# Kernel optimization log

Measured on AMD Instinct MI355X. Metric: run time of the kernel, lower is better.

## Reference

```python
import jax, jax.numpy as jnp
import numpy as np

B, T, D = 128, 1024, 128
HS = [100, 100, 200, 200]  # stacked LSTM hidden sizes (from initialize_carry calls)
OUT = 6


def _lstm_layer(xs, Wx, Wh, b):
    """Flax-style LSTMCell scanned over time. xs: [B,T,Din] -> [B,T,H].
    Gates: i,f,g,o ; c' = sig(f)*c + sig(i)*tanh(g) ; h' = sig(o)*tanh(c')."""
    Bsz = xs.shape[0]
    H = Wh.shape[0]
    c0 = jnp.zeros((Bsz, H), xs.dtype)
    h0 = jnp.zeros((Bsz, H), xs.dtype)

    def step(carry, x_t):
        c, h = carry
        z = x_t @ Wx + h @ Wh + b  # [B, 4H]
        i, f, g, o = jnp.split(z, 4, axis=-1)
        c = jax.nn.sigmoid(f) * c + jax.nn.sigmoid(i) * jnp.tanh(g)
        h = jax.nn.sigmoid(o) * jnp.tanh(c)
        return (c, h), h

    (_, _), hs = jax.lax.scan(step, (c0, h0), jnp.swapaxes(xs, 0, 1))  # hs: [T,B,H]
    return jnp.swapaxes(hs, 0, 1)


def setup_inputs() -> dict:
    key = jax.random.key(0)
    ks = jax.random.split(key, 16)
    xs = jax.random.normal(ks[0], (B, T, D), dtype=jnp.float32)
    inp = {"xs": xs}
    d_in = D
    for li, H in enumerate(HS):
        s_x = 1.0 / np.sqrt(d_in)
        s_h = 1.0 / np.sqrt(H)
        inp[f"Wx{li}"] = jax.random.normal(ks[1 + 3 * li], (d_in, 4 * H), dtype=jnp.float32) * s_x
        inp[f"Wh{li}"] = jax.random.normal(ks[2 + 3 * li], (H, 4 * H), dtype=jnp.float32) * s_h
        inp[f"b{li}"] = jnp.zeros((4 * H,), dtype=jnp.float32)
        d_in = H
    inp["Wd"] = jax.random.normal(ks[13], (HS[-1], OUT), dtype=jnp.float32) / np.sqrt(HS[-1])
    inp["bd"] = jnp.zeros((OUT,), dtype=jnp.float32)
    return inp


def reference(xs, Wx0, Wh0, b0, Wx1, Wh1, b1, Wx2, Wh2, b2, Wx3, Wh3, b3, Wd, bd):
    # Four stacked scanned LSTM layers (dropout is identity in eval mode)
    h = _lstm_layer(xs, Wx0, Wh0, b0)
    h = _lstm_layer(h, Wx1, Wh1, b1)
    h = _lstm_layer(h, Wx2, Wh2, b2)
    h = _lstm_layer(h, Wx3, Wh3, b3)
    last = h[:, -1, :]  # [B, 200]
    return last @ Wd + bd  # [B, 6]
```

## Files before the change

### kernel.cpp

```cpp
#include <hip/hip_runtime.h>
#include <cstdint>
#include <cstddef>


#define AGENT __HIP_MEMORY_SCOPE_AGENT
#define FSTR 64

typedef __attribute__((ext_vector_type(8))) short  short8;
typedef __attribute__((ext_vector_type(4))) float  f32x4;

struct us4 { unsigned short x, y, z, w; };

__device__ __forceinline__ unsigned short f2bf(float x){
  unsigned u = __float_as_uint(x);
  unsigned r = u + 0x7FFFu + ((u >> 16) & 1u);
  return (unsigned short)(r >> 16);
}
__device__ __forceinline__ float bf2f(unsigned short h){
  return __uint_as_float(((unsigned)h) << 16);
}
__device__ __forceinline__ float sigmoidf_(float x){ return 1.f / (1.f + __expf(-x)); }

__device__ __forceinline__ void spin_ge(const unsigned* p, unsigned v){
  #pragma unroll 1
  for (int i = 0; i < 32; ++i){
    if (__hip_atomic_load(p, __ATOMIC_RELAXED, AGENT) >= v) return;
  }
  long s = 0;
  #pragma unroll 1
  while (__hip_atomic_load(p, __ATOMIC_RELAXED, AGENT) < v){
    __builtin_amdgcn_s_sleep(8);
    if (++s > (1L << 17)) break;
  }
}

__device__ __forceinline__ void load_hx(const unsigned* base, int w32, int loOff,
                                        short8& ah, short8& al){
  union U { unsigned long long q[2]; short8 v; } uh, ul;
  const unsigned long long* ph = (const unsigned long long*)(base + w32);
  const unsigned long long* pl = (const unsigned long long*)(base + loOff + w32);
  uh.q[0] = __hip_atomic_load(ph + 0, __ATOMIC_RELAXED, AGENT);
  uh.q[1] = __hip_atomic_load(ph + 1, __ATOMIC_RELAXED, AGENT);
  ul.q[0] = __hip_atomic_load(pl + 0, __ATOMIC_RELAXED, AGENT);
  ul.q[1] = __hip_atomic_load(pl + 1, __ATOMIC_RELAXED, AGENT);
  ah = uh.v; al = ul.v;
}

__global__ __launch_bounds__(256) void gemm_pregate(
    const float* __restrict__ A, const float* __restrict__ W,
    const float* __restrict__ bias, float* __restrict__ G,
    int K, int KT, int N, size_t strideT, size_t strideB)
{
  __shared__ unsigned short Ahi[256*40];
  __shared__ unsigned short Alo[256*40];
  __shared__ unsigned short Bhi[80*40];
  __shared__ unsigned short Blo[80*40];

  const int tid  = threadIdx.x;
  const int mb   = blockIdx.x;
  const int n0   = blockIdx.y * 80;
  const int wave = tid >> 6, lane = tid & 63;
  const int ln15 = lane & 15, quad = lane >> 4;

  f32x4 acc[4][5];
  for (int a = 0; a < 4; ++a)
    for (int b = 0; b < 5; ++b)
      acc[a][b] = (f32x4){0.f, 0.f, 0.f, 0.f};

  for (int kt = 0; kt < KT; ++kt){
    const int k0 = kt * 32;
    const bool full = (k0 + 31) < K;
    for (int i = 0; i < 8; ++i){
      const int e   = tid + 256*i;
      const int row = e >> 3, seg = e & 7;
      const int mm  = mb*256 + row;
      const float* rp = A + (size_t)(mm >> 7)*strideT + (size_t)(mm & 127)*strideB;
      const int k = k0 + seg*4;
      float v0, v1, v2, v3;
      if (full){
        float4 v = *(const float4*)(rp + k);
        v0 = v.x; v1 = v.y; v2 = v.z; v3 = v.w;
      } else {
        v0 = (k+0 < K) ? rp[k+0] : 0.f;
        v1 = (k+1 < K) ? rp[k+1] : 0.f;
        v2 = (k+2 < K) ? rp[k+2] : 0.f;
        v3 = (k+3 < K) ? rp[k+3] : 0.f;
      }
      const unsigned short h0=f2bf(v0), h1=f2bf(v1), h2=f2bf(v2), h3=f2bf(v3);
      us4 hv{h0, h1, h2, h3};
      us4 lv{f2bf(v0-bf2f(h0)), f2bf(v1-bf2f(h1)), f2bf(v2-bf2f(h2)), f2bf(v3-bf2f(h3))};
      *(us4*)&Ahi[row*40 + seg*4] = hv;
      *(us4*)&Alo[row*40 + seg*4] = lv;
    }
    for (int i = 0; i < 10; ++i){
      const int e  = tid + 256*i;
      const int kk = e / 80, nn = e - kk*80;
      const int k  = k0 + kk;
      const float v = (k < K) ? W[(size_t)k*N + n0 + nn] : 0.f;
      const unsigned short hb = f2bf(v);
      Bhi[nn*40 + kk] = hb;
      Blo[nn*40 + kk] = f2bf(v - bf2f(hb));
    }
    __syncthreads();
    short8 a_h[4], a_l[4];
    for (int mt = 0; mt < 4; ++mt){
      const int aoff = (wave*64 + mt*16 + ln15)*40 + quad*8;
      a_h[mt] = *(const short8*)&Ahi[aoff];
      a_l[mt] = *(const short8*)&Alo[aoff];
    }
    for (int nt = 0; nt < 5; ++nt){
      const int boff = (nt*16 + ln15)*40 + quad*8;
      const short8 b_h = *(const short8*)&Bhi[boff];
      const short8 b_l = *(const short8*)&Blo[boff];
      for (int mt = 0; mt < 4; ++mt){
        acc[mt][nt] = __builtin_amdgcn_mfma_f32_16x16x32_bf16(a_h[mt], b_h, acc[mt][nt], 0,0,0);
        acc[mt][nt] = __builtin_amdgcn_mfma_f32_16x16x32_bf16(a_l[mt], b_h, acc[mt][nt], 0,0,0);
        acc[mt][nt] = __builtin_amdgcn_mfma_f32_16x16x32_bf16(a_h[mt], b_l, acc[mt][nt], 0,0,0);
      }
    }
    __syncthreads();
  }
  for (int nt = 0; nt < 5; ++nt){
    const float bv = bias[n0 + nt*16 + ln15];
    for (int mt = 0; mt < 4; ++mt){
      const int mbase = mb*256 + wave*64 + mt*16 + quad*4;
      #pragma unroll
      for (int r = 0; r < 4; ++r)
        G[(size_t)(mbase + r)*N + n0 + nt*16 + ln15] = acc[mt][nt][r] + bv;
    }
  }
}

template<int H, int HP, int P, bool HAS_X>
__device__ __forceinline__ void rec_stage(
    const float* __restrict__ G0, const float* __restrict__ Wx,
    const float* __restrict__ Wh, const float* __restrict__ bias,
    int HprevReal,
    const unsigned* __restrict__ HxUp, unsigned* __restrict__ HxOwn,
    const unsigned* __restrict__ flgUp, unsigned* __restrict__ flgOwn,
    unsigned* __restrict__ flgDn, int PUp, int PDn,
    float* __restrict__ cstate, float* __restrict__ hlast,
    int g, int m, int t0, int TC, int Tlast, char* smem)
{
  constexpr int HHM  = H / P;
  constexpr int COLS = 4 * HHM;
  constexpr int CP   = COLS;
  constexpr int ZSTR = CP + 1;
  constexpr int KPo  = ((H + 31)/32)*32;
  constexpr int RSo  = KPo / 2;
  constexpr int RSp  = HP / 2;
  constexpr int KX   = HAS_X ? HP : 0;
  constexpr int KALL = KX + KPo;
  constexpr int KTX  = KX / 32;
  constexpr int KTH  = KPo / 32;
  constexpr int KSTR = KALL + 8;
  constexpr int NT   = CP / 16;
  constexpr int NE   = 16 * HHM / 2;
  constexpr int PR   = HHM / 2;
  constexpr int N4H  = 4 * H;
  constexpr int SLOTo = 2*16*RSo;
  constexpr int SLOTp = 2*16*RSp;

  unsigned short* whT_hi = (unsigned short*)smem;
  unsigned short* whT_lo = whT_hi + CP*KSTR;
  float* zbuf = (float*)(whT_lo + CP*KSTR);

  const int tid  = threadIdx.x;
  const int row0 = g * 16;
  const int lane = tid & 63, wave = tid >> 6;
  const int ln15 = lane & 15, quad = lane >> 4;

  for (int e = tid; e < COLS*KALL; e += 256){
    const int k = e / COLS, c = e - k*COLS;
    const int gate = c / HHM, hh = c - gate*HHM;
    const int col = gate*H + m*HHM + hh;
    float w = 0.f;
    if (HAS_X){
      if (k < KX){ if (k < HprevReal) w = Wx[(size_t)k*N4H + col]; }
      else { const int k2 = k - KX; if (k2 < H) w = Wh[(size_t)k2*N4H + col]; }
    } else {
      if (k < H) w = Wh[(size_t)k*N4H + col];
    }
    const unsigned short hi = f2bf(w);
    whT_hi[c*KSTR + k] = hi;
    whT_lo[c*KSTR + k] = f2bf(w - bf2f(hi));
  }

  const int r_g  = tid / PR;
  const int hh0  = 2*(tid - r_g*PR);
  const int kidx = m*HHM + hh0;
  float c0 = 0.f, c1 = 0.f;
  if (tid < NE && t0 > 0){
    const float2 cv = *(const float2*)&cstate[(size_t)(row0 + r_g)*H + kidx];
    c0 = cv.x; c1 = cv.y;
  }
  float2 bv[4] = {};
  if (HAS_X){
    if (tid < NE){
      #pragma unroll
      for (int gate = 0; gate < 4; ++gate)
        bv[gate] = *(const float2*)&bias[gate*H + kidx];
    }
  }
  __syncthreads();

  const int g16 = g*16;

  for (int tl = 0; tl < TC; ++tl){
    const int t = t0 + tl;

    float2 gv[4] = {};
    if constexpr (!HAS_X){
      if (tid < NE){
        const float* Gt = G0 + ((size_t)tl*128 + row0 + r_g)*(size_t)N4H + kidx;
        #pragma unroll
        for (int gate = 0; gate < 4; ++gate)
          gv[gate] = *(const float2*)(Gt + gate*H);
      }
    }

    if (HAS_X && wave == 0 && lane < PUp)
      spin_ge(&flgUp[(size_t)(g16 + lane)*FSTR], (unsigned)(t+1));
    if (PDn > 0 && t >= 8 && wave == 1 && lane < PDn)
      spin_ge(&flgDn[(size_t)(g16 + lane)*FSTR], (unsigned)(t-7));
    __syncthreads();

    f32x4 acc[2];
    acc[0] = (f32x4){0.f,0.f,0.f,0.f};
    acc[1] = (f32x4){0.f,0.f,0.f,0.f};
    auto do_tile = [&](const short8& a_h, const short8& a_l, int koW){
      #pragma unroll
      for (int s = 0; s < 2; ++s){
        const int nt = wave + 4*s;
        if (nt < NT){
          const int boff = (nt*16 + ln15)*KSTR + quad*8 + koW;
          const short8 b_h = *(const short8*)&whT_hi[boff];
          const short8 b_l = *(const short8*)&whT_lo[boff];
          acc[s] = __builtin_amdgcn_mfma_f32_16x16x32_bf16(a_h, b_h, acc[s], 0,0,0);
          acc[s] = __builtin_amdgcn_mfma_f32_16x16x32_bf16(a_l, b_h, acc[s], 0,0,0);
          acc[s] = __builtin_amdgcn_mfma_f32_16x16x32_bf16(a_h, b_l, acc[s], 0,0,0);
        }
      }
    };

    if constexpr (HAS_X){
      const unsigned* up = HxUp + ((size_t)(t & 7)*8 + g) * SLOTp;
      #pragma unroll
      for (int kt = 0; kt < KTX; ++kt){
        short8 a_h, a_l;
        load_hx(up, ln15*RSp + kt*16 + quad*4, 16*RSp, a_h, a_l);
        do_tile(a_h, a_l, kt*32);
      }
    }

    if (wave == 0 && lane < P)
      spin_ge(&flgOwn[(size_t)(g16 + lane)*FSTR], (unsigned)t);
    __syncthreads();

    {
      const unsigned* own = HxOwn + ((size_t)((t-1) & 7)*8 + g) * SLOTo;
      #pragma unroll
      for (int kt = 0; kt < KTH; ++kt){
        short8 a_h, a_l;
        load_hx(own, ln15*RSo + kt*16 + quad*4, 16*RSo, a_h, a_l);
        do_tile(a_h, a_l, KX + kt*32);
      }
    }
    {
      #pragma unroll
      for (int s = 0; s < 2; ++s){
        const int nt = wave + 4*s;
        if (nt < NT)
          #pragma unroll
          for (int r = 0; r < 4; ++r)
            zbuf[(quad*4 + r)*ZSTR + nt*16 + ln15] = acc[s][r];
      }
    }
    __syncthreads();

    if (tid < NE){
      const float* zr = zbuf + r_g*ZSTR;
      const float2 b0 = HAS_X ? bv[0] : gv[0];
      const float2 b1 = HAS_X ? bv[1] : gv[1];
      const float2 b2 = HAS_X ? bv[2] : gv[2];
      const float2 b3 = HAS_X ? bv[3] : gv[3];
      const float zi0 = zr[0*HHM + hh0]   + b0.x, zi1 = zr[0*HHM + hh0+1] + b0.y;
      const float zf0 = zr[1*HHM + hh0]   + b1.x, zf1 = zr[1*HHM + hh0+1] + b1.y;
      const float zg0 = zr[2*HHM + hh0]   + b2.x, zg1 = zr[2*HHM + hh0+1] + b2.y;
      const float zo0 = zr[3*HHM + hh0]   + b3.x, zo1 = zr[3*HHM + hh0+1] + b3.y;
      c0 = sigmoidf_(zf0)*c0 + sigmoidf_(zi0)*tanhf(zg0);
      c1 = sigmoidf_(zf1)*c1 + sigmoidf_(zi1)*tanhf(zg1);
      const float h0 = sigmoidf_(zo0)*tanhf(c0);
      const float h1 = sigmoidf_(zo1)*tanhf(c1);
      const unsigned short h0h = f2bf(h0), h1h = f2bf(h1);
      const unsigned short h0l = f2bf(h0 - bf2f(h0h)), h1l = f2bf(h1 - bf2f(h1h));
      const unsigned whi = ((unsigned)h1h << 16) | (unsigned)h0h;
      const unsigned wlo = ((unsigned)h1l << 16) | (unsigned)h0l;
      unsigned* dst = HxOwn + ((size_t)(t & 7)*8 + g) * SLOTo;
      const int w32 = r_g*RSo + (kidx >> 1);
      __hip_atomic_store(&dst[w32],          whi, __ATOMIC_RELAXED, AGENT);
      __hip_atomic_store(&dst[16*RSo + w32], wlo, __ATOMIC_RELAXED, AGENT);
      if (hlast && t == Tlast-1){
        float2 hv{h0, h1};
        *(float2*)&hlast[(size_t)(row0 + r_g)*H + kidx] = hv;
      }
    }
    __syncthreads();
    if (tid == 0)
      __hip_atomic_store(&flgOwn[(size_t)(g16 + m)*FSTR], (unsigned)(t+1),
                         __ATOMIC_RELAXED, AGENT);
  }

  if (tid < NE){
    float2 cv{c0, c1};
    *(float2*)&cstate[(size_t)(row0 + r_g)*H + kidx] = cv;
  }
}

struct FusedArgs {
  const float *G0;
  const float *Wx1, *Wx2, *Wx3;
  const float *Wh0, *Wh1, *Wh2, *Wh3;
  const float *b1, *b2, *b3;
  unsigned *Hx0, *Hx1, *Hx2, *Hx3;
  unsigned *flags;
  float *cst;
  float *hlast;
  int t0, TC, Tlast;
};

__global__ __launch_bounds__(256) void lstm_fused(FusedArgs a){
  extern __shared__ char smem[];
  const int b = blockIdx.x;
  constexpr int LF = 128*FSTR;
  if (b < 40){
    rec_stage<100, 0, 5, false>(a.G0, nullptr, a.Wh0, nullptr, 0,
        nullptr, a.Hx0, nullptr, a.flags + 0*LF, a.flags + 1*LF, 0, 5,
        a.cst + 0*128*200, nullptr, b & 7, b >> 3, a.t0, a.TC, a.Tlast, smem);
  } else if (b < 80){
    const int bb = b - 40;
    rec_stage<100, 128, 5, true>(nullptr, a.Wx1, a.Wh1, a.b1, 100,
        a.Hx0, a.Hx1, a.flags + 0*LF, a.flags + 1*LF, a.flags + 2*LF, 5, 10,
        a.cst + 1*128*200, nullptr, bb & 7, bb >> 3, a.t0, a.TC, a.Tlast, smem);
  } else if (b < 160){
    const int bb = b - 80;
    rec_stage<200, 128, 10, true>(nullptr, a.Wx2, a.Wh2, a.b2, 100,
        a.Hx1, a.Hx2, a.flags + 1*LF, a.flags + 2*LF, a.flags + 3*LF, 5, 10,
        a.cst + 2*128*200, nullptr, bb & 7, bb >> 3, a.t0, a.TC, a.Tlast, smem);
  } else {
    const int bb = b - 160;
    rec_stage<200, 224, 10, true>(nullptr, a.Wx3, a.Wh3, a.b3, 200,
        a.Hx2, a.Hx3, a.flags + 2*LF, a.flags + 3*LF, nullptr, 10, 0,
        a.cst + 3*128*200, a.hlast, bb & 7, bb >> 3, a.t0, a.TC, a.Tlast, smem);
  }
}

__global__ __launch_bounds__(256) void head_kernel(
    const float* __restrict__ hlast, const float* __restrict__ Wd,
    const float* __restrict__ bd, float* __restrict__ out)
{
  const int e = blockIdx.x*256 + threadIdx.x;
  if (e >= 128*6) return;
  const int b = e / 6, o = e - 6*b;
  float s = bd[o];
  const float* hp = hlast + (size_t)b*200;
  for (int k = 0; k < 200; ++k) s += hp[k] * Wd[k*6 + o];
  out[e] = s;
}

__global__ void fill_sentinel(float* out, int n){
  const int i = blockIdx.x*blockDim.x + threadIdx.x;
  if (i < n) out[i] = 1.0e30f;
}

extern "C" void kernel_launch(void* const* d_in, const int* in_sizes, int n_in,
                              void* d_out, int out_size, void* d_ws, size_t ws_size,
                              hipStream_t stream)
{
  (void)in_sizes; (void)n_in;
  const float* xs  = (const float*)d_in[0];
  const float* Wx[4] = {(const float*)d_in[1], (const float*)d_in[4],
                        (const float*)d_in[7], (const float*)d_in[10]};
  const float* Wh[4] = {(const float*)d_in[2], (const float*)d_in[5],
                        (const float*)d_in[8], (const float*)d_in[11]};
  const float* bs[4] = {(const float*)d_in[3], (const float*)d_in[6],
                        (const float*)d_in[9], (const float*)d_in[12]};
  const float* Wd = (const float*)d_in[13];
  const float* bd = (const float*)d_in[14];
  float* out = (float*)d_out;

  char* ws = (char*)d_ws;
  const size_t HXU[4] = {131072, 131072, 229376, 229376};
  const size_t HX_TOT = HXU[0]+HXU[1]+HXU[2]+HXU[3];
  const size_t FLAGS_BYTES = (size_t)4*128*FSTR*4;
  size_t off = 0;
  const size_t OFF_FLAGS = off; off += FLAGS_BYTES;
  const size_t OFF_HX    = off; off += HX_TOT*4;
  const size_t OFF_CST   = off; off += (size_t)4*128*200*4;
  const size_t OFF_HLAST = off; off += (size_t)128*200*4;
  off = (off + 255) & ~(size_t)255;
  const size_t FIXED_END = off;

  int CT = 0;
  for (int ct = 1024; ct >= 8; ct >>= 1){
    const size_t need = FIXED_END + (size_t)ct*128*400*4;
    if (ws_size >= need){ CT = ct; break; }
  }
  if (CT == 0){
    fill_sentinel<<<(out_size + 255)/256, 256, 0, stream>>>(out, out_size);
    return;
  }

  unsigned* flags = (unsigned*)(ws + OFF_FLAGS);
  unsigned* Hx0   = (unsigned*)(ws + OFF_HX);
  unsigned* Hx1   = Hx0 + HXU[0];
  unsigned* Hx2   = Hx1 + HXU[1];
  unsigned* Hx3   = Hx2 + HXU[2];
  float* cst      = (float*)(ws + OFF_CST);
  float* hlast    = (float*)(ws + OFF_HLAST);
  float* G0       = (float*)(ws + FIXED_END);

  const int FUSED_LDS = 151104;
  hipFuncSetAttribute(reinterpret_cast<const void*>(lstm_fused),
                      hipFuncAttributeMaxDynamicSharedMemorySize, FUSED_LDS);

  hipMemsetAsync(flags, 0, FLAGS_BYTES, stream);
  hipMemsetAsync(Hx0, 0, HX_TOT*4, stream);

  FusedArgs fa;
  fa.Wx1 = Wx[1]; fa.Wx2 = Wx[2]; fa.Wx3 = Wx[3];
  fa.Wh0 = Wh[0]; fa.Wh1 = Wh[1]; fa.Wh2 = Wh[2]; fa.Wh3 = Wh[3];
  fa.b1 = bs[1];  fa.b2 = bs[2];  fa.b3 = bs[3];
  fa.Hx0 = Hx0; fa.Hx1 = Hx1; fa.Hx2 = Hx2; fa.Hx3 = Hx3;
  fa.flags = flags; fa.cst = cst; fa.hlast = hlast;
  fa.G0 = G0; fa.Tlast = 1024;

  const int NC  = 1024 / CT;
  const int GMX = CT*128/256;
  for (int c = 0; c < NC; ++c){
    const int t0 = c*CT;
    gemm_pregate<<<dim3(GMX,5), 256, 0, stream>>>(xs + (size_t)t0*128, Wx[0], bs[0], G0,
        128, 4, 400, (size_t)128, (size_t)131072);
    fa.t0 = t0; fa.TC = CT;
    lstm_fused<<<240, 256, FUSED_LDS, stream>>>(fa);
  }

  head_kernel<<<3, 256, 0, stream>>>(hlast, Wd, bd, out);
}
```

Baseline: 6.527 ms.

## Split input projections of layers 1-3 into separate producer blocks

Adds dedicated pre_stage blocks that compute the Wx input projection plus bias for layers 1-3 into ring-buffered gate arrays. The recurrent blocks then only do the Wh matmul on the critical path, which shortens each serial timestep. Flag waits are spread across individual lanes with an acquire fence in place of __syncthreads, and the new flags signal to producers when ring slots can be reused. Block count rises from 240 to 440 and the LDS request is reduced so all blocks stay co-resident. The cost is extra global traffic for the gate arrays and more spin-wait synchronisation, with a deadlock risk if the blocks are not all resident at once.

```diff
diff --git a/kernel.cpp b/kernel.cpp
--- a/kernel.cpp
+++ b/kernel.cpp
@@ -131,56 +131,42 @@
   }
 }
 
-template<int H, int HP, int P, bool HAS_X>
-__device__ __forceinline__ void rec_stage(
-    const float* __restrict__ G0, const float* __restrict__ Wx,
-    const float* __restrict__ Wh, const float* __restrict__ bias,
-    int HprevReal,
-    const unsigned* __restrict__ HxUp, unsigned* __restrict__ HxOwn,
-    const unsigned* __restrict__ flgUp, unsigned* __restrict__ flgOwn,
-    unsigned* __restrict__ flgDn, int PUp, int PDn,
+template<int H, int P, bool GW>
+__device__ __forceinline__ void rec_stage2(
+    const float* __restrict__ Gsrc, const float* __restrict__ Wh,
+    unsigned* __restrict__ HxOwn,
+    unsigned* __restrict__ flgOwn, const unsigned* __restrict__ flgG,
+    const unsigned* __restrict__ flgDn, int PDn,
     float* __restrict__ cstate, float* __restrict__ hlast,
     int g, int m, int t0, int TC, int Tlast, char* smem)
 {
   constexpr int HHM  = H / P;
   constexpr int COLS = 4 * HHM;
-  constexpr int CP   = COLS;
-  constexpr int ZSTR = CP + 1;
+  constexpr int ZSTR = COLS + 1;
   constexpr int KPo  = ((H + 31)/32)*32;
   constexpr int RSo  = KPo / 2;
-  constexpr int RSp  = HP / 2;
-  constexpr int KX   = HAS_X ? HP : 0;
-  constexpr int KALL = KX + KPo;
-  constexpr int KTX  = KX / 32;
   constexpr int KTH  = KPo / 32;
-  constexpr int KSTR = KALL + 8;
-  constexpr int NT   = CP / 16;
+  constexpr int KSTR = KPo + 8;
+  constexpr int NT   = COLS / 16;
   constexpr int NE   = 16 * HHM / 2;
   constexpr int PR   = HHM / 2;
   constexpr int N4H  = 4 * H;
   constexpr int SLOTo = 2*16*RSo;
-  constexpr int SLOTp = 2*16*RSp;
 
   unsigned short* whT_hi = (unsigned short*)smem;
-  unsigned short* whT_lo = whT_hi + CP*KSTR;
-  float* zbuf = (float*)(whT_lo + CP*KSTR);
+  unsigned short* whT_lo = whT_hi + COLS*KSTR;
+  float* zbuf = (float*)(whT_lo + COLS*KSTR);
 
   const int tid  = threadIdx.x;
   const int row0 = g * 16;
   const int lane = tid & 63, wave = tid >> 6;
   const int ln15 = lane & 15, quad = lane >> 4;
 
-  for (int e = tid; e < COLS*KALL; e += 256){
+  for (int e = tid; e < COLS*KPo; e += 256){
     const int k = e / COLS, c = e - k*COLS;
     const int gate = c / HHM, hh = c - gate*HHM;
     const int col = gate*H + m*HHM + hh;
-    float w = 0.f;
-    if (HAS_X){
-      if (k < KX){ if (k < HprevReal) w = Wx[(size_t)k*N4H + col]; }
-      else { const int k2 = k - KX; if (k2 < H) w = Wh[(size_t)k2*N4H + col]; }
-    } else {
-      if (k < H) w = Wh[(size_t)k*N4H + col];
-    }
+    float w = (k < H) ? Wh[(size_t)k*N4H + col] : 0.f;
     const unsigned short hi = f2bf(w);
     whT_hi[c*KSTR + k] = hi;
     whT_lo[c*KSTR + k] = f2bf(w - bf2f(hi));
@@ -194,14 +180,6 @@
     const float2 cv = *(const float2*)&cstate[(size_t)(row0 + r_g)*H + kidx];
     c0 = cv.x; c1 = cv.y;
   }
-  float2 bv[4] = {};
-  if (HAS_X){
-    if (tid < NE){
-      #pragma unroll
-      for (int gate = 0; gate < 4; ++gate)
-        bv[gate] = *(const float2*)&bias[gate*H + kidx];
-    }
-  }
   __syncthreads();
 
   const int g16 = g*16;
@@ -209,85 +187,67 @@
   for (int tl = 0; tl < TC; ++tl){
     const int t = t0 + tl;
 
-    float2 gv[4] = {};
-    if constexpr (!HAS_X){
-      if (tid < NE){
-        const float* Gt = G0 + ((size_t)tl*128 + row0 + r_g)*(size_t)N4H + kidx;
-        #pragma unroll
-        for (int gate = 0; gate < 4; ++gate)
-          gv[gate] = *(const float2*)(Gt + gate*H);
-      }
-    }
-
-    if (HAS_X && wave == 0 && lane < PUp)
-      spin_ge(&flgUp[(size_t)(g16 + lane)*FSTR], (unsigned)(t+1));
-    if (PDn > 0 && t >= 8 && wave == 1 && lane < PDn)
-      spin_ge(&flgDn[(size_t)(g16 + lane)*FSTR], (unsigned)(t-7));
-    __syncthreads();
+    if (lane < P && lane != m)
+      spin_ge(&flgOwn[(size_t)(g16 + lane)*FSTR], (unsigned)t);
+    if (PDn > 0 && t >= 8 && lane >= 40 && lane < 40 + PDn)
+      spin_ge(&flgDn[(size_t)(g16 + (lane-40))*FSTR], (unsigned)(t-7));
+    if (GW && lane == 62)
+      spin_ge(&flgG[(size_t)(g16 + m)*FSTR], (unsigned)(t+1));
+    __builtin_amdgcn_fence(__ATOMIC_ACQUIRE, "agent");
+
+    float2 gv[4];
+    if (tid < NE){
+      const float* Gt = GW
+          ? Gsrc + ((size_t)(t & 7)*128 + row0 + r_g)*(size_t)N4H + kidx
+          : Gsrc + ((size_t)tl*128 + row0 + r_g)*(size_t)N4H + kidx;
+      #pragma unroll
+      for (int gate = 0; gate < 4; ++gate){
+        union { unsigned long long q; float2 f; } u;
+        u.q = __hip_atomic_load((const unsigned long long*)(Gt + gate*H),
+                                __ATOMIC_RELAXED, AGENT);
+        gv[gate] = u.f;
+      }
+    }
 
     f32x4 acc[2];
     acc[0] = (f32x4){0.f,0.f,0.f,0.f};
     acc[1] = (f32x4){0.f,0.f,0.f,0.f};
-    auto do_tile = [&](const short8& a_h, const short8& a_l, int koW){
-      #pragma unroll
-      for (int s = 0; s < 2; ++s){
-        const int nt = wave + 4*s;
-        if (nt < NT){
-          const int boff = (nt*16 + ln15)*KSTR + quad*8 + koW;
-          const short8 b_h = *(const short8*)&whT_hi[boff];
-          const short8 b_l = *(const short8*)&whT_lo[boff];
-          acc[s] = __builtin_amdgcn_mfma_f32_16x16x32_bf16(a_h, b_h, acc[s], 0,0,0);
-          acc[s] = __builtin_amdgcn_mfma_f32_16x16x32_bf16(a_l, b_h, acc[s], 0,0,0);
-          acc[s] = __builtin_amdgcn_mfma_f32_16x16x32_bf16(a_h, b_l, acc[s], 0,0,0);
-        }
-      }
-    };
-
-    if constexpr (HAS_X){
-      const unsigned* up = HxUp + ((size_t)(t & 7)*8 + g) * SLOTp;
-      #pragma unroll
-      for (int kt = 0; kt < KTX; ++kt){
-        short8 a_h, a_l;
-        load_hx(up, ln15*RSp + kt*16 + quad*4, 16*RSp, a_h, a_l);
-        do_tile(a_h, a_l, kt*32);
-      }
-    }
-
-    if (wave == 0 && lane < P)
-      spin_ge(&flgOwn[(size_t)(g16 + lane)*FSTR], (unsigned)t);
-    __syncthreads();
-
     {
       const unsigned* own = HxOwn + ((size_t)((t-1) & 7)*8 + g) * SLOTo;
       #pragma unroll
       for (int kt = 0; kt < KTH; ++kt){
         short8 a_h, a_l;
         load_hx(own, ln15*RSo + kt*16 + quad*4, 16*RSo, a_h, a_l);
-        do_tile(a_h, a_l, KX + kt*32);
-      }
-    }
-    {
-      #pragma unroll
-      for (int s = 0; s < 2; ++s){
-        const int nt = wave + 4*s;
-        if (nt < NT)
-          #pragma unroll
-          for (int r = 0; r < 4; ++r)
-            zbuf[(quad*4 + r)*ZSTR + nt*16 + ln15] = acc[s][r];
-      }
+        #pragma unroll
+        for (int s = 0; s < 2; ++s){
+          const int nt = wave + 4*s;
+          if (nt < NT){
+            const int boff = (nt*16 + ln15)*KSTR + quad*8 + kt*32;
+            const short8 b_h = *(const short8*)&whT_hi[boff];
+            const short8 b_l = *(const short8*)&whT_lo[boff];
+            acc[s] = __builtin_amdgcn_mfma_f32_16x16x32_bf16(a_h, b_h, acc[s], 0,0,0);
+            acc[s] = __builtin_amdgcn_mfma_f32_16x16x32_bf16(a_l, b_h, acc[s], 0,0,0);
+            acc[s] = __builtin_amdgcn_mfma_f32_16x16x32_bf16(a_h, b_l, acc[s], 0,0,0);
+          }
+        }
+      }
+    }
+    #pragma unroll
+    for (int s = 0; s < 2; ++s){
+      const int nt = wave + 4*s;
+      if (nt < NT)
+        #pragma unroll
+        for (int r = 0; r < 4; ++r)
+          zbuf[(quad*4 + r)*ZSTR + nt*16 + ln15] = acc[s][r];
     }
     __syncthreads();
 
     if (tid < NE){
       const float* zr = zbuf + r_g*ZSTR;
-      const float2 b0 = HAS_X ? bv[0] : gv[0];
-      const float2 b1 = HAS_X ? bv[1] : gv[1];
-      const float2 b2 = HAS_X ? bv[2] : gv[2];
-      const float2 b3 = HAS_X ? bv[3] : gv[3];
-      const float zi0 = zr[0*HHM + hh0]   + b0.x, zi1 = zr[0*HHM + hh0+1] + b0.y;
-      const float zf0 = zr[1*HHM + hh0]   + b1.x, zf1 = zr[1*HHM + hh0+1] + b1.y;
-      const float zg0 = zr[2*HHM + hh0]   + b2.x, zg1 = zr[2*HHM + hh0+1] + b2.y;
-      const float zo0 = zr[3*HHM + hh0]   + b3.x, zo1 = zr[3*HHM + hh0+1] + b3.y;
+      const float zi0 = zr[0*HHM + hh0]   + gv[0].x, zi1 = zr[0*HHM + hh0+1] + gv[0].y;
+      const float zf0 = zr[1*HHM + hh0]   + gv[1].x, zf1 = zr[1*HHM + hh0+1] + gv[1].y;
+      const float zg0 = zr[2*HHM + hh0]   + gv[2].x, zg1 = zr[2*HHM + hh0+1] + gv[2].y;
+      const float zo0 = zr[3*HHM + hh0]   + gv[3].x, zo1 = zr[3*HHM + hh0+1] + gv[3].y;
       c0 = sigmoidf_(zf0)*c0 + sigmoidf_(zi0)*tanhf(zg0);
       c1 = sigmoidf_(zf1)*c1 + sigmoidf_(zi1)*tanhf(zg1);
       const float h0 = sigmoidf_(zo0)*tanhf(c0);
@@ -317,12 +277,110 @@
   }
 }
 
+template<int H, int P, int HP, int Pprev>
+__device__ __forceinline__ void pre_stage(
+    const float* __restrict__ Wx, const float* __restrict__ bias, int HprevReal,
+    const unsigned* __restrict__ HxUp, float* __restrict__ Gdst,
+    const unsigned* __restrict__ flgUp, const unsigned* __restrict__ flgRec,
+    unsigned* __restrict__ flgPre,
+    int g, int m, int t0, int TC, char* smem)
+{
+  constexpr int HHM  = H / P;
+  constexpr int COLS = 4 * HHM;
+  constexpr int KSTR = HP + 8;
+  constexpr int KTX  = HP / 32;
+  constexpr int NT   = COLS / 16;
+  constexpr int N4H  = 4 * H;
+  constexpr int RSp  = HP / 2;
+  constexpr int SLOTp = 2*16*RSp;
+
+  unsigned short* wxT_hi = (unsigned short*)smem;
+  unsigned short* wxT_lo = wxT_hi + COLS*KSTR;
+
+  const int tid  = threadIdx.x;
+  const int lane = tid & 63, wave = tid >> 6;
+  const int ln15 = lane & 15, quad = lane >> 4;
+  const int g16  = g*16;
+
+  for (int e = tid; e < COLS*HP; e += 256){
+    const int k = e / COLS, c = e - k*COLS;
+    const int gate = c / HHM, hh = c - gate*HHM;
+    const int col = gate*H + m*HHM + hh;
+    float w = (k < HprevReal) ? Wx[(size_t)k*N4H + col] : 0.f;
+    const unsigned short hi = f2bf(w);
+    wxT_hi[c*KSTR + k] = hi;
+    wxT_lo[c*KSTR + k] = f2bf(w - bf2f(hi));
+  }
+
+  int cN[2]; float bN[2];
+  #pragma unroll
+  for (int s = 0; s < 2; ++s){
+    const int nt = wave + 4*s;
+    if (nt < NT){
+      const int sc = nt*16 + ln15;
+      const int gate = sc / HHM, hh = sc - gate*HHM;
+      cN[s] = gate*H + m*HHM + hh;
+      bN[s] = bias[cN[s]];
+    } else { cN[s] = 0; bN[s] = 0.f; }
+  }
+  __syncthreads();
+
+  for (int tl = 0; tl < TC; ++tl){
+    const int t = t0 + tl;
+
+    if (lane < Pprev)
+      spin_ge(&flgUp[(size_t)(g16 + lane)*FSTR], (unsigned)(t+1));
+    if (t >= 8 && lane == 62)
+      spin_ge(&flgRec[(size_t)(g16 + m)*FSTR], (unsigned)(t-7));
+    __builtin_amdgcn_fence(__ATOMIC_ACQUIRE, "agent");
+
+    f32x4 acc[2];
+    acc[0] = (f32x4){0.f,0.f,0.f,0.f};
+    acc[1] = (f32x4){0.f,0.f,0.f,0.f};
+    const unsigned* up = HxUp + ((size_t)(t & 7)*8 + g) * SLOTp;
+    #pragma unroll
+    for (int kt = 0; kt < KTX; ++kt){
+      short8 a_h, a_l;
+      load_hx(up, ln15*RSp + kt*16 + quad*4, 16*RSp, a_h, a_l);
+      #pragma unroll
+      for (int s = 0; s < 2; ++s){
+        const int nt = wave + 4*s;
+        if (nt < NT){
+          const int boff = (nt*16 + ln15)*KSTR + quad*8 + kt*32;
+          const short8 b_h = *(const short8*)&wxT_hi[boff];
+          const short8 b_l = *(const short8*)&wxT_lo[boff];
+          acc[s] = __builtin_amdgcn_mfma_f32_16x16x32_bf16(a_h, b_h, acc[s], 0,0,0);
+          acc[s] = __builtin_amdgcn_mfma_f32_16x16x32_bf16(a_l, b_h, acc[s], 0,0,0);
+          acc[s] = __builtin_amdgcn_mfma_f32_16x16x32_bf16(a_h, b_l, acc[s], 0,0,0);
+        }
+      }
+    }
+
+    const size_t rbase = ((size_t)(t & 7)*128 + g16 + quad*4);
+    #pragma unroll
+    for (int s = 0; s < 2; ++s){
+      const int nt = wave + 4*s;
+      if (nt < NT){
+        #pragma unroll
+        for (int r = 0; r < 4; ++r)
+          __hip_atomic_store(&Gdst[(rbase + r)*N4H + cN[s]], acc[s][r] + bN[s],
+                             __ATOMIC_RELAXED, AGENT);
+      }
+    }
+    __syncthreads();
+    if (tid == 0)
+      __hip_atomic_store(&flgPre[(size_t)(g16 + m)*FSTR], (unsigned)(t+1),
+                         __ATOMIC_RELAXED, AGENT);
+  }
+}
+
 struct FusedArgs {
   const float *G0;
   const float *Wx1, *Wx2, *Wx3;
   const float *Wh0, *Wh1, *Wh2, *Wh3;
   const float *b1, *b2, *b3;
   unsigned *Hx0, *Hx1, *Hx2, *Hx3;
+  float *G1, *G2, *G3;
   unsigned *flags;
   float *cst;
   float *hlast;
@@ -333,25 +391,38 @@
   extern __shared__ char smem[];
   const int b = blockIdx.x;
   constexpr int LF = 128*FSTR;
+  unsigned* F = a.flags;
   if (b < 40){
-    rec_stage<100, 0, 5, false>(a.G0, nullptr, a.Wh0, nullptr, 0,
-        nullptr, a.Hx0, nullptr, a.flags + 0*LF, a.flags + 1*LF, 0, 5,
+    rec_stage2<100, 5, false>(a.G0, a.Wh0, a.Hx0,
+        F + 0*LF, nullptr, F + 4*LF, 5,
         a.cst + 0*128*200, nullptr, b & 7, b >> 3, a.t0, a.TC, a.Tlast, smem);
   } else if (b < 80){
     const int bb = b - 40;
-    rec_stage<100, 128, 5, true>(nullptr, a.Wx1, a.Wh1, a.b1, 100,
-        a.Hx0, a.Hx1, a.flags + 0*LF, a.flags + 1*LF, a.flags + 2*LF, 5, 10,
+    rec_stage2<100, 5, true>(a.G1, a.Wh1, a.Hx1,
+        F + 1*LF, F + 4*LF, F + 5*LF, 10,
         a.cst + 1*128*200, nullptr, bb & 7, bb >> 3, a.t0, a.TC, a.Tlast, smem);
   } else if (b < 160){
     const int bb = b - 80;
-    rec_stage<200, 128, 10, true>(nullptr, a.Wx2, a.Wh2, a.b2, 100,
-        a.Hx1, a.Hx2, a.flags + 1*LF, a.flags + 2*LF, a.flags + 3*LF, 5, 10,
+    rec_stage2<200, 10, true>(a.G2, a.Wh2, a.Hx2,
+        F + 2*LF, F + 5*LF, F + 6*LF, 10,
         a.cst + 2*128*200, nullptr, bb & 7, bb >> 3, a.t0, a.TC, a.Tlast, smem);
+  } else if (b < 240){
+    const int bb = b - 160;
+    rec_stage2<200, 10, true>(a.G3, a.Wh3, a.Hx3,
+        F + 3*LF, F + 6*LF, nullptr, 0,
+        a.cst + 3*128*200, a.hlast, bb & 7, bb >> 3, a.t0, a.TC, a.Tlast, smem);
+  } else if (b < 280){
+    const int bb = b - 240;
+    pre_stage<100, 5, 128, 5>(a.Wx1, a.b1, 100, a.Hx0, a.G1,
+        F + 0*LF, F + 1*LF, F + 4*LF, bb & 7, bb >> 3, a.t0, a.TC, smem);
+  } else if (b < 360){
+    const int bb = b - 280;
+    pre_stage<200, 10, 128, 5>(a.Wx2, a.b2, 100, a.Hx1, a.G2,
+        F + 1*LF, F + 2*LF, F + 5*LF, bb & 7, bb >> 3, a.t0, a.TC, smem);
   } else {
-    const int bb = b - 160;
-    rec_stage<200, 224, 10, true>(nullptr, a.Wx3, a.Wh3, a.b3, 200,
-        a.Hx2, a.Hx3, a.flags + 2*LF, a.flags + 3*LF, nullptr, 10, 0,
-        a.cst + 3*128*200, a.hlast, bb & 7, bb >> 3, a.t0, a.TC, a.Tlast, smem);
+    const int bb = b - 360;
+    pre_stage<200, 10, 224, 10>(a.Wx3, a.b3, 200, a.Hx2, a.G3,
+        F + 2*LF, F + 3*LF, F + 6*LF, bb & 7, bb >> 3, a.t0, a.TC, smem);
   }
 }
 
@@ -392,10 +463,14 @@
   char* ws = (char*)d_ws;
   const size_t HXU[4] = {131072, 131072, 229376, 229376};
   const size_t HX_TOT = HXU[0]+HXU[1]+HXU[2]+HXU[3];
-  const size_t FLAGS_BYTES = (size_t)4*128*FSTR*4;
+  const size_t FLAGS_BYTES = (size_t)7*128*FSTR*4;
+  const size_t G1U = (size_t)8*128*400;
+  const size_t G2U = (size_t)8*128*800;
+  const size_t G3U = (size_t)8*128*800;
   size_t off = 0;
   const size_t OFF_FLAGS = off; off += FLAGS_BYTES;
   const size_t OFF_HX    = off; off += HX_TOT*4;
+  const size_t OFF_G     = off; off += (G1U+G2U+G3U)*4;
   const size_t OFF_CST   = off; off += (size_t)4*128*200*4;
   const size_t OFF_HLAST = off; off += (size_t)128*200*4;
   off = (off + 255) & ~(size_t)255;
@@ -416,11 +491,14 @@
   unsigned* Hx1   = Hx0 + HXU[0];
   unsigned* Hx2   = Hx1 + HXU[1];
   unsigned* Hx3   = Hx2 + HXU[2];
+  float* G1       = (float*)(ws + OFF_G);
+  float* G2       = G1 + G1U;
+  float* G3       = G2 + G2U;
   float* cst      = (float*)(ws + OFF_CST);
   float* hlast    = (float*)(ws + OFF_HLAST);
   float* G0       = (float*)(ws + FIXED_END);
 
-  const int FUSED_LDS = 151104;
+  const int FUSED_LDS = 79424;
   hipFuncSetAttribute(reinterpret_cast<const void*>(lstm_fused),
                       hipFuncAttributeMaxDynamicSharedMemorySize, FUSED_LDS);
 
@@ -432,6 +510,7 @@
   fa.Wh0 = Wh[0]; fa.Wh1 = Wh[1]; fa.Wh2 = Wh[2]; fa.Wh3 = Wh[3];
   fa.b1 = bs[1];  fa.b2 = bs[2];  fa.b3 = bs[3];
   fa.Hx0 = Hx0; fa.Hx1 = Hx1; fa.Hx2 = Hx2; fa.Hx3 = Hx3;
+  fa.G1 = G1; fa.G2 = G2; fa.G3 = G3;
   fa.flags = flags; fa.cst = cst; fa.hlast = hlast;
   fa.G0 = G0; fa.Tlast = 1024;
 
@@ -442,7 +521,7 @@
     gemm_pregate<<<dim3(GMX,5), 256, 0, stream>>>(xs + (size_t)t0*128, Wx[0], bs[0], G0,
         128, 4, 400, (size_t)128, (size_t)131072);
     fa.t0 = t0; fa.TC = CT;
-    lstm_fused<<<240, 256, FUSED_LDS, stream>>>(fa);
+    lstm_fused<<<440, 256, FUSED_LDS, stream>>>(fa);
   }
 
   head_kernel<<<3, 256, 0, stream>>>(hlast, Wd, bd, out);
```

Result: slower. 18.84 ms (+188.7%).
